# Optimization experiments

Measured on AMD Instinct MI355X. Metric: run time of the kernel, lower is better.

The kernel has to match this reference:

```python
import jax, jax.numpy as jnp
import numpy as np

P_DROP = 0.2
NEG_SLOPE = 0.2


def setup_inputs() -> dict:
    key = jax.random.key(0)
    ks = jax.random.split(key, 12)
    N, E = 50000, 800000
    IN, H1, H2, OUT = 256, 256, 128, 64
    x = jax.random.normal(ks[0], (N, IN), dtype=jnp.float32)
    adj_rows = jax.random.randint(ks[1], (E,), 0, N, dtype=jnp.int32)
    adj_cols = jax.random.randint(ks[2], (E,), 0, N, dtype=jnp.int32)
    adj_vals = jax.random.uniform(ks[3], (E,), dtype=jnp.float32)
    W1 = jax.random.normal(ks[4], (H1, IN), dtype=jnp.float32) * (1.0 / np.sqrt(IN))
    b1 = jax.random.normal(ks[5], (H1,), dtype=jnp.float32) * 0.01
    W2 = jax.random.normal(ks[6], (H2, H1), dtype=jnp.float32) * (1.0 / np.sqrt(H1))
    b2 = jax.random.normal(ks[7], (H2,), dtype=jnp.float32) * 0.01
    W3 = jax.random.normal(ks[8], (OUT, H2), dtype=jnp.float32) * (1.0 / np.sqrt(H2))
    b3 = jax.random.normal(ks[9], (OUT,), dtype=jnp.float32) * 0.01
    mask1 = jax.random.bernoulli(ks[10], 1.0 - P_DROP, (N, H1))
    mask2 = jax.random.bernoulli(ks[11], 1.0 - P_DROP, (N, H2))
    return {"x": x, "adj_rows": adj_rows, "adj_cols": adj_cols, "adj_vals": adj_vals,
            "W1": W1, "b1": b1, "W2": W2, "b2": b2, "W3": W3, "b3": b3,
            "mask1": mask1, "mask2": mask2}


def _spmm(rows, cols, vals, h, n_nodes):
    # sparse adjacency matmul: out[r] = sum_e vals[e] * h[cols[e]] for rows[e]==r
    msgs = vals[:, None] * h[cols]  # [E, d] irregular gather
    return jax.ops.segment_sum(msgs, rows, num_segments=n_nodes)


def _gcn_layer(x, W, b, rows, cols, vals, n_nodes):
    h = x @ W.T + b  # nn.Linear
    return _spmm(rows, cols, vals, h, n_nodes)


def reference(x, adj_rows, adj_cols, adj_vals, W1, b1, W2, b2, W3, b3, mask1, mask2):
    N = x.shape[0]
    keep = 1.0 / (1.0 - P_DROP)
    h = _gcn_layer(x, W1, b1, adj_rows, adj_cols, adj_vals, N)
    h = jnp.where(h >= 0, h, NEG_SLOPE * h)
    h = jnp.where(mask1, h * keep, 0.0)
    h = _gcn_layer(h, W2, b2, adj_rows, adj_cols, adj_vals, N)
    h = jnp.where(h >= 0, h, NEG_SLOPE * h)
    h = jnp.where(mask2, h * keep, 0.0)
    z = _gcn_layer(h, W3, b3, adj_rows, adj_cols, adj_vals, N)
    return z
```

## Files before the change

kernel.cpp:

```cpp
#include <hip/hip_runtime.h>


typedef unsigned short ushort_t;
typedef __attribute__((ext_vector_type(8))) short bf16x8;
typedef __attribute__((ext_vector_type(4))) float f32x4;
typedef __attribute__((ext_vector_type(2))) unsigned int u32x2;

__device__ __forceinline__ float bf2f(ushort_t u) {
  return __uint_as_float(((unsigned int)u) << 16);
}
__device__ __forceinline__ ushort_t f2bf(float f) {
  unsigned int u = __float_as_uint(f);
  return (ushort_t)((u + 0x7FFFu + ((u >> 16) & 1u)) >> 16);
}
__device__ __forceinline__ float read_f(const void* p, int fm, size_t i) {
  return fm ? bf2f(((const ushort_t*)p)[i]) : ((const float*)p)[i];
}

__device__ __forceinline__ bool mask_keep(const void* mask, int mm, size_t o) {
  switch (mm) {
    case 1:  return ((const int*)mask)[o] != 0;
    case 2:  return ((const unsigned int*)mask)[o] != 0u;
    case 3:  return ((const ushort_t*)mask)[o] != 0;
    default: return ((const unsigned char*)mask)[o] != 0;
  }
}

__global__ void prep_kernel(const void* __restrict__ x,
                            const void* __restrict__ m1,
                            const void* __restrict__ m2,
                            int* __restrict__ modes,
                            int* __restrict__ zero_region, int zn) {
  if (blockIdx.x == 0) {
    __shared__ int bfok;
    if (threadIdx.x == 0) bfok = 1;
    __syncthreads();
    for (int i = threadIdx.x; i < 8192; i += blockDim.x) {
      ushort_t h = ((const ushort_t*)x)[i];
      int e = (h >> 7) & 0xFF;
      if (!(h == 0 || (e >= 95 && e <= 133))) atomicAnd(&bfok, 0);
    }
    __syncthreads();
    if (threadIdx.x == 0) modes[0] = bfok;
  } else if (blockIdx.x <= 2) {
    const void* p = (blockIdx.x == 1) ? m1 : m2;
    __shared__ int ok[4];
    if (threadIdx.x < 4) ok[threadIdx.x] = 1;
    __syncthreads();
    for (int i = threadIdx.x; i < 4096; i += blockDim.x) {
      unsigned int w = ((const unsigned int*)p)[i];
      if (!(w == 0u || w == 1u)) atomicAnd(&ok[0], 0);
      if (!(w == 0u || w == 0x3F800000u)) atomicAnd(&ok[1], 0);
      unsigned int h16 = w >> 16, l16 = w & 0xFFFFu;
      if (!((h16 == 0u || h16 == 0x3F80u) && (l16 == 0u || l16 == 0x3F80u)))
        atomicAnd(&ok[2], 0);
      if (((w | (w >> 8) | (w >> 16) | (w >> 24)) & 0xFEu) != 0u) atomicAnd(&ok[3], 0);
    }
    __syncthreads();
    if (threadIdx.x == 0)
      modes[blockIdx.x] = ok[0] ? 1 : (ok[1] ? 2 : (ok[2] ? 3 : 0));
  } else {
    int i = (blockIdx.x - 3) * blockDim.x + threadIdx.x;
    int stride = (gridDim.x - 3) * blockDim.x;
    for (; i < zn; i += stride) zero_region[i] = 0;
  }
}

__global__ void hist_kernel(const int* __restrict__ rows, int* __restrict__ cnt, int E) {
  int i = blockIdx.x * blockDim.x + threadIdx.x;
  int stride = gridDim.x * blockDim.x;
  for (; i < E; i += stride) atomicAdd(&cnt[rows[i]], 1);
}

__global__ void scan_part_kernel(const int* __restrict__ cnt, int* __restrict__ part, int n) {
  __shared__ int s[256];
  int i = blockIdx.x * 256 + threadIdx.x;
  s[threadIdx.x] = (i < n) ? cnt[i] : 0;
  __syncthreads();
  for (int off = 128; off > 0; off >>= 1) {
    if (threadIdx.x < off) s[threadIdx.x] += s[threadIdx.x + off];
    __syncthreads();
  }
  if (threadIdx.x == 0) part[blockIdx.x] = s[0];
}

__global__ __launch_bounds__(1024) void scan_top_kernel(int* __restrict__ part, int P) {
  __shared__ int s[1024];
  int t = threadIdx.x;
  int v = (t < P) ? part[t] : 0;
  s[t] = v;
  __syncthreads();
  for (int off = 1; off < 1024; off <<= 1) {
    int x = s[t];
    int y = (t >= off) ? s[t - off] : 0;
    __syncthreads();
    s[t] = x + y;
    __syncthreads();
  }
  if (t < P) part[t] = s[t] - v;
}

__global__ void scan_apply_kernel(const int* __restrict__ cnt, const int* __restrict__ part,
                                  int* __restrict__ row_start, int n) {
  __shared__ int s[256];
  int base = part[blockIdx.x];
  int i = blockIdx.x * 256 + threadIdx.x;
  int v = (i < n) ? cnt[i] : 0;
  s[threadIdx.x] = v;
  __syncthreads();
  for (int off = 1; off < 256; off <<= 1) {
    int x = s[threadIdx.x];
    int y = (threadIdx.x >= off) ? s[threadIdx.x - off] : 0;
    __syncthreads();
    s[threadIdx.x] = x + y;
    __syncthreads();
  }
  if (i < n) row_start[i] = base + s[threadIdx.x] - v;
  if (i == n - 1) row_start[n] = base + s[threadIdx.x];
}

__global__ void scatter_kernel(const int* __restrict__ rows, const int* __restrict__ cols,
                               const void* __restrict__ vals, const int* __restrict__ fm_p,
                               const int* __restrict__ row_start, int* __restrict__ fill,
                               int2* __restrict__ ecv, int E) {
  int fm = *fm_p;
  int i = blockIdx.x * blockDim.x + threadIdx.x;
  int stride = gridDim.x * blockDim.x;
  for (; i < E; i += stride) {
    int r = rows[i];
    int pos = atomicAdd(&fill[r], 1);
    int idx = row_start[r] + pos;
    ecv[idx] = make_int2(cols[i], __float_as_int(read_f(vals, fm, i)));
  }
}

__global__ void convert_all_kernel(
    const void* __restrict__ W1, const void* __restrict__ W2, const void* __restrict__ W3,
    const void* __restrict__ b1, const void* __restrict__ b2, const void* __restrict__ b3,
    const void* __restrict__ x, const int* __restrict__ fm_p,
    ushort_t* __restrict__ whi, ushort_t* __restrict__ wlo,
    float* __restrict__ biasf, ushort_t* __restrict__ xbf,
    int n1, int n2, int n3, int h1, int h2, int h3, int nx4) {
  int fm = *fm_p;
  int wtot = n1 + n2 + n3;
  int btot = h1 + h2 + h3;
  int total = wtot + btot + nx4;
  int i = blockIdx.x * blockDim.x + threadIdx.x;
  int stride = gridDim.x * blockDim.x;
  for (; i < total; i += stride) {
    if (i < wtot) {
      const void* src; int j;
      if (i < n1) { src = W1; j = i; }
      else if (i < n1 + n2) { src = W2; j = i - n1; }
      else { src = W3; j = i - n1 - n2; }
      float v = read_f(src, fm, j);
      ushort_t h = f2bf(v);
      whi[i] = h;
      wlo[i] = f2bf(v - bf2f(h));
    } else if (i < wtot + btot) {
      int k = i - wtot;
      const void* src; int j;
      if (k < h1) { src = b1; j = k; }
      else if (k < h1 + h2) { src = b2; j = k - h1; }
      else { src = b3; j = k - h1 - h2; }
      biasf[k] = read_f(src, fm, j);
    } else {
      int k = i - wtot - btot;
      if (fm == 0) {
        f32x4 v = ((const f32x4*)x)[k];
        unsigned int lo = (unsigned int)f2bf(v[0]) | ((unsigned int)f2bf(v[1]) << 16);
        unsigned int hi = (unsigned int)f2bf(v[2]) | ((unsigned int)f2bf(v[3]) << 16);
        ((u32x2*)xbf)[k] = (u32x2){lo, hi};
      } else {
        ((u32x2*)xbf)[k] = ((const u32x2*)x)[k];
      }
    }
  }
}

template<int KC>
__global__ __launch_bounds__(256) void gemm_breg_kernel(
    const ushort_t* __restrict__ A,
    const ushort_t* __restrict__ Whi, const ushort_t* __restrict__ Wlo,
    const float* __restrict__ bias, ushort_t* __restrict__ g, int ldg,
    int M, int nct) {
  const int K = KC * 32;
  int wave = threadIdx.x >> 6, lane = threadIdx.x & 63;
  int gw = blockIdx.x * 4 + wave;
  int NW = gridDim.x * 4;
  int mr = lane & 15, quad = lane >> 4;
  int ct = gw % nct;
  int nrt = (M + 15) >> 4;
  int ntasks = nct * nrt;
  if (gw >= ntasks) return;

  bf16x8 wh[KC], wl[KC];
  {
    const ushort_t* wp = Whi + (size_t)(ct * 16 + mr) * K + quad * 8;
    const ushort_t* wq = Wlo + (size_t)(ct * 16 + mr) * K + quad * 8;
#pragma unroll
    for (int kc = 0; kc < KC; ++kc) {
      wh[kc] = *(const bf16x8*)(wp + kc * 32);
      wl[kc] = *(const bf16x8*)(wq + kc * 32);
    }
  }
  int col = ct * 16 + mr;
  float bv = bias[col];

  int task = gw;
  bf16x8 af[KC];
  {
    int m = (task / nct) * 16 + mr; if (m >= M) m = M - 1;
    const ushort_t* ap = A + (size_t)m * K + quad * 8;
#pragma unroll
    for (int kc = 0; kc < KC; ++kc) af[kc] = *(const bf16x8*)(ap + kc * 32);
  }

#pragma unroll 1
  for (;;) {
    int next = task + NW;
    bool has_next = next < ntasks;
    bf16x8 afn[KC];
    if (has_next) {
      int m = (next / nct) * 16 + mr; if (m >= M) m = M - 1;
      const ushort_t* ap = A + (size_t)m * K + quad * 8;
#pragma unroll
      for (int kc = 0; kc < KC; ++kc) afn[kc] = *(const bf16x8*)(ap + kc * 32);
    }

    f32x4 acc[4];
#pragma unroll
    for (int t = 0; t < 4; ++t) acc[t] = (f32x4){0.f, 0.f, 0.f, 0.f};
#pragma unroll
    for (int kc = 0; kc < KC; ++kc) {
      acc[(2 * kc) & 3] = __builtin_amdgcn_mfma_f32_16x16x32_bf16(af[kc], wh[kc], acc[(2 * kc) & 3], 0, 0, 0);
      acc[(2 * kc + 1) & 3] = __builtin_amdgcn_mfma_f32_16x16x32_bf16(af[kc], wl[kc], acc[(2 * kc + 1) & 3], 0, 0, 0);
    }
    int m0 = (task / nct) * 16;
#pragma unroll
    for (int r = 0; r < 4; ++r) {
      int row = m0 + quad * 4 + r;
      float s = ((acc[0][r] + acc[1][r]) + (acc[2][r] + acc[3][r])) + bv;
      if (row < M) g[(size_t)row * ldg + col] = f2bf(s);
    }
    if (!has_next) break;
#pragma unroll
    for (int kc = 0; kc < KC; ++kc) af[kc] = afn[kc];
    task = next;
  }
}

template<int MODE, int VEC>
__global__ __launch_bounds__(256) void spmm7_kernel(
    const int* __restrict__ row_start, const int2* __restrict__ ecv,
    const ushort_t* __restrict__ G, int D,
    const void* __restrict__ mask, const int* __restrict__ mmode_p,
    void* __restrict__ outp, int N) {
  int wave = threadIdx.x >> 6, lane = threadIdx.x & 63;
  int r = blockIdx.x * 4 + wave;
  if (r >= N) return;
  int f0 = lane * VEC;
  int e  = __builtin_amdgcn_readfirstlane(row_start[r]);
  int e1 = __builtin_amdgcn_readfirstlane(row_start[r + 1]);
  float a[VEC];
#pragma unroll
  for (int q = 0; q < VEC; ++q) a[q] = 0.f;

  for (; e + 8 <= e1; e += 8) {
    int2 cv[8];
#pragma unroll
    for (int j = 0; j < 8; ++j) cv[j] = ecv[e + j];
    if (VEC == 4) {
      u32x2 gg[8];
#pragma unroll
      for (int j = 0; j < 8; ++j)
        gg[j] = *(const u32x2*)(G + (size_t)cv[j].x * D + f0);
#pragma unroll
      for (int j = 0; j < 8; ++j) {
        float v = __int_as_float(cv[j].y);
        a[0] += v * bf2f((ushort_t)gg[j][0]);
        a[1] += v * bf2f((ushort_t)(gg[j][0] >> 16));
        a[2] += v * bf2f((ushort_t)gg[j][1]);
        a[3] += v * bf2f((ushort_t)(gg[j][1] >> 16));
      }
    } else if (VEC == 2) {
      unsigned int gg[8];
#pragma unroll
      for (int j = 0; j < 8; ++j)
        gg[j] = *(const unsigned int*)(G + (size_t)cv[j].x * D + f0);
#pragma unroll
      for (int j = 0; j < 8; ++j) {
        float v = __int_as_float(cv[j].y);
        a[0] += v * bf2f((ushort_t)gg[j]);
        a[1] += v * bf2f((ushort_t)(gg[j] >> 16));
      }
    } else {
      ushort_t h[8];
#pragma unroll
      for (int j = 0; j < 8; ++j) h[j] = G[(size_t)cv[j].x * D + f0];
#pragma unroll
      for (int j = 0; j < 8; ++j) a[0] += __int_as_float(cv[j].y) * bf2f(h[j]);
    }
  }
  if (e < e1) {
    int idx[8]; float v[8];
#pragma unroll
    for (int j = 0; j < 8; ++j) {
      int ee = e + j;
      bool ok = ee < e1;
      int2 cv = ecv[ok ? ee : e1 - 1];
      idx[j] = cv.x;
      v[j] = ok ? __int_as_float(cv.y) : 0.f;
    }
    if (VEC == 4) {
      u32x2 gg[8];
#pragma unroll
      for (int j = 0; j < 8; ++j)
        gg[j] = *(const u32x2*)(G + (size_t)idx[j] * D + f0);
#pragma unroll
      for (int j = 0; j < 8; ++j) {
        a[0] += v[j] * bf2f((ushort_t)gg[j][0]);
        a[1] += v[j] * bf2f((ushort_t)(gg[j][0] >> 16));
        a[2] += v[j] * bf2f((ushort_t)gg[j][1]);
        a[3] += v[j] * bf2f((ushort_t)(gg[j][1] >> 16));
      }
    } else if (VEC == 2) {
      unsigned int gg[8];
#pragma unroll
      for (int j = 0; j < 8; ++j)
        gg[j] = *(const unsigned int*)(G + (size_t)idx[j] * D + f0);
#pragma unroll
      for (int j = 0; j < 8; ++j) {
        a[0] += v[j] * bf2f((ushort_t)gg[j]);
        a[1] += v[j] * bf2f((ushort_t)(gg[j] >> 16));
      }
    } else {
      ushort_t h[8];
#pragma unroll
      for (int j = 0; j < 8; ++j) h[j] = G[(size_t)idx[j] * D + f0];
#pragma unroll
      for (int j = 0; j < 8; ++j) a[0] += v[j] * bf2f(h[j]);
    }
  }

  size_t o = (size_t)r * D + f0;
  if (MODE == 1) {
    int mm = *mmode_p;
    ushort_t pk[VEC];
#pragma unroll
    for (int q = 0; q < VEC; ++q) {
      float t = a[q];
      t = (t >= 0.f) ? t : 0.2f * t;
      t = mask_keep(mask, mm, o + q) ? t * 1.25f : 0.f;
      pk[q] = f2bf(t);
    }
    if (VEC == 4) {
      u32x2 w;
      w[0] = (unsigned int)pk[0] | ((unsigned int)pk[1] << 16);
      w[1] = (unsigned int)pk[2] | ((unsigned int)pk[3] << 16);
      *(u32x2*)((ushort_t*)outp + o) = w;
    } else if (VEC == 2) {
      *(unsigned int*)((ushort_t*)outp + o) =
          (unsigned int)pk[0] | ((unsigned int)pk[1] << 16);
    } else {
      ((ushort_t*)outp)[o] = pk[0];
    }
  } else {
#pragma unroll
    for (int q = 0; q < VEC; ++q) ((float*)outp)[o + q] = a[q];
  }
}

extern "C" void kernel_launch(void* const* d_in, const int* in_sizes, int n_in,
                              void* d_out, int out_size, void* d_ws, size_t ws_size,
                              hipStream_t stream) {
  const void* x     = d_in[0];
  const int*  rows  = (const int*)d_in[1];
  const int*  cols  = (const int*)d_in[2];
  const void* vals  = d_in[3];
  const void* W1    = d_in[4];
  const void* b1    = d_in[5];
  const void* W2    = d_in[6];
  const void* b2    = d_in[7];
  const void* W3    = d_in[8];
  const void* b3    = d_in[9];
  const void* mask1 = d_in[10];
  const void* mask2 = d_in[11];

  const int H1  = in_sizes[5];
  const int H2  = in_sizes[7];
  const int OUT = in_sizes[9];
  const int IN  = in_sizes[4] / H1;
  const int N   = in_sizes[0] / IN;
  const int E   = in_sizes[1];
  const int W1n = in_sizes[4], W2n = in_sizes[6], W3n = in_sizes[8];

  char* ws = (char*)d_ws;
  size_t off = 0;
  auto alloc = [&](size_t bytes) -> void* {
    void* p = ws + off;
    off = (off + bytes + 255) & ~(size_t)255;
    return p;
  };
  int*      modes     = (int*)alloc(4 * 4);
  int*      row_start = (int*)alloc((size_t)(N + 1) * 4);
  int*      cnt       = (int*)alloc((size_t)N * 8);
  int*      part      = (int*)alloc(1024 * 4);
  int2*     ecv       = (int2*)alloc((size_t)E * 8);
  ushort_t* whi       = (ushort_t*)alloc((size_t)(W1n + W2n + W3n) * 2);
  ushort_t* wlo       = (ushort_t*)alloc((size_t)(W1n + W2n + W3n) * 2);
  float*    biasf     = (float*)alloc((size_t)(H1 + H2 + OUT) * 4);
  ushort_t* bufA      = (ushort_t*)alloc((size_t)N * H1 * 2);
  ushort_t* bufB      = (ushort_t*)alloc((size_t)N * H1 * 2);
  ushort_t* bufC      = (ushort_t*)alloc((size_t)N * H1 * 2);

  int* fmode = modes;
  int* mm1   = modes + 1;
  int* mm2   = modes + 2;
  int* fill  = cnt + N;
  ushort_t* w1hi = whi,             *w1lo = wlo;
  ushort_t* w2hi = whi + W1n,       *w2lo = wlo + W1n;
  ushort_t* w3hi = whi + W1n + W2n, *w3lo = wlo + W1n + W2n;

  prep_kernel<<<259, 256, 0, stream>>>(x, mask1, mask2, modes, cnt, 2 * N);

  const int P = (N + 255) / 256;
  hist_kernel<<<1024, 256, 0, stream>>>(rows, cnt, E);
  scan_part_kernel<<<P, 256, 0, stream>>>(cnt, part, N);
  scan_top_kernel<<<1, 1024, 0, stream>>>(part, P);
  scan_apply_kernel<<<P, 256, 0, stream>>>(cnt, part, row_start, N);
  scatter_kernel<<<1024, 256, 0, stream>>>(rows, cols, vals, fmode, row_start, fill, ecv, E);

  convert_all_kernel<<<2048, 256, 0, stream>>>(
      W1, W2, W3, b1, b2, b3, x, fmode, whi, wlo, biasf, bufA,
      W1n, W2n, W3n, H1, H2, OUT, (N * IN) / 4);

  const int GEMM_BLOCKS = 1024;
  int spmm_grid = (N + 3) / 4;

  gemm_breg_kernel<8><<<GEMM_BLOCKS, 256, 0, stream>>>(
      bufA, w1hi, w1lo, biasf, bufB, H1, N, H1 / 16);
  spmm7_kernel<1, 4><<<spmm_grid, 256, 0, stream>>>(
      row_start, ecv, bufB, H1, mask1, mm1, bufC, N);
  gemm_breg_kernel<8><<<GEMM_BLOCKS, 256, 0, stream>>>(
      bufC, w2hi, w2lo, biasf + H1, bufB, H2, N, H2 / 16);
  spmm7_kernel<1, 2><<<spmm_grid, 256, 0, stream>>>(
      row_start, ecv, bufB, H2, mask2, mm2, bufA, N);
  gemm_breg_kernel<4><<<GEMM_BLOCKS, 256, 0, stream>>>(
      bufA, w3hi, w3lo, biasf + H1 + H2, bufB, OUT, N, OUT / 16);
  spmm7_kernel<0, 1><<<spmm_grid, 256, 0, stream>>>(
      row_start, ecv, bufB, OUT, nullptr, fmode, d_out, N);
}
```

Baseline: 477.9 us.

## Store GEMM operands in MFMA fragment-major layout for contiguous wave loads

Weights, the converted input and the SpMM outputs that feed the next GEMM are now written in a fragment-tiled layout (16-row blocks, 32-wide k chunks), so each wave loads a whole bf16x8 fragment as one contiguous 1 KB span instead of strided row reads. This is meant to make GEMM A/W loads fully coalesced. The cost is scattered, less coalesced writes in the convert and SpMM epilogues, and buffers padded to a multiple of 16 rows. Padding rows are never written, so GEMM reads uninitialised data there, but those rows are discarded at store time.

```diff
diff --git a/kernel.cpp b/kernel.cpp
--- a/kernel.cpp
+++ b/kernel.cpp
@@ -15,6 +15,11 @@
 }
 __device__ __forceinline__ float read_f(const void* p, int fm, size_t i) {
   return fm ? bf2f(((const ushort_t*)p)[i]) : ((const float*)p)[i];
+}
+
+__device__ __forceinline__ size_t frag_off(int m, int k, int K) {
+  return (size_t)(m >> 4) * 16 * K + ((size_t)(k >> 5) << 9) +
+         (((k >> 3) & 3) << 7) + ((m & 15) << 3) + (k & 7);
 }
 
 __device__ __forceinline__ bool mask_keep(const void* mask, int mm, size_t o) {
@@ -140,23 +145,26 @@
     const void* __restrict__ x, const int* __restrict__ fm_p,
     ushort_t* __restrict__ whi, ushort_t* __restrict__ wlo,
     float* __restrict__ biasf, ushort_t* __restrict__ xbf,
-    int n1, int n2, int n3, int h1, int h2, int h3, int nx4) {
+    int n1, int n2, int n3, int h1, int h2, int h3, int K1, int K2, int K3, int nx) {
   int fm = *fm_p;
   int wtot = n1 + n2 + n3;
   int btot = h1 + h2 + h3;
+  int nx4 = nx / 4;
   int total = wtot + btot + nx4;
   int i = blockIdx.x * blockDim.x + threadIdx.x;
   int stride = gridDim.x * blockDim.x;
   for (; i < total; i += stride) {
     if (i < wtot) {
-      const void* src; int j;
-      if (i < n1) { src = W1; j = i; }
-      else if (i < n1 + n2) { src = W2; j = i - n1; }
-      else { src = W3; j = i - n1 - n2; }
+      const void* src; int j, K; size_t base;
+      if (i < n1) { src = W1; j = i; K = K1; base = 0; }
+      else if (i < n1 + n2) { src = W2; j = i - n1; K = K2; base = n1; }
+      else { src = W3; j = i - n1 - n2; K = K3; base = (size_t)n1 + n2; }
+      int n = j / K, k = j - n * K;
       float v = read_f(src, fm, j);
       ushort_t h = f2bf(v);
-      whi[i] = h;
-      wlo[i] = f2bf(v - bf2f(h));
+      size_t o = base + frag_off(n, k, K);
+      whi[o] = h;
+      wlo[o] = f2bf(v - bf2f(h));
     } else if (i < wtot + btot) {
       int k = i - wtot;
       const void* src; int j;
@@ -165,15 +173,21 @@
       else { src = b3; j = k - h1 - h2; }
       biasf[k] = read_f(src, fm, j);
     } else {
-      int k = i - wtot - btot;
+      int k4 = i - wtot - btot;
+      int m = k4 / (K1 / 4);
+      int k0 = (k4 - m * (K1 / 4)) * 4;
+      ushort_t p0, p1, p2, p3;
       if (fm == 0) {
-        f32x4 v = ((const f32x4*)x)[k];
-        unsigned int lo = (unsigned int)f2bf(v[0]) | ((unsigned int)f2bf(v[1]) << 16);
-        unsigned int hi = (unsigned int)f2bf(v[2]) | ((unsigned int)f2bf(v[3]) << 16);
-        ((u32x2*)xbf)[k] = (u32x2){lo, hi};
+        f32x4 v = ((const f32x4*)x)[k4];
+        p0 = f2bf(v[0]); p1 = f2bf(v[1]); p2 = f2bf(v[2]); p3 = f2bf(v[3]);
       } else {
-        ((u32x2*)xbf)[k] = ((const u32x2*)x)[k];
+        const ushort_t* xb = (const ushort_t*)x + (size_t)k4 * 4;
+        p0 = xb[0]; p1 = xb[1]; p2 = xb[2]; p3 = xb[3];
       }
+      size_t o = frag_off(m, k0, K1);
+      *(u32x2*)(xbf + o) = (u32x2){
+          (unsigned int)p0 | ((unsigned int)p1 << 16),
+          (unsigned int)p2 | ((unsigned int)p3 << 16)};
     }
   }
 }
@@ -196,12 +210,12 @@
 
   bf16x8 wh[KC], wl[KC];
   {
-    const ushort_t* wp = Whi + (size_t)(ct * 16 + mr) * K + quad * 8;
-    const ushort_t* wq = Wlo + (size_t)(ct * 16 + mr) * K + quad * 8;
+    const ushort_t* wp = Whi + (size_t)ct * 16 * K + lane * 8;
+    const ushort_t* wq = Wlo + (size_t)ct * 16 * K + lane * 8;
 #pragma unroll
     for (int kc = 0; kc < KC; ++kc) {
-      wh[kc] = *(const bf16x8*)(wp + kc * 32);
-      wl[kc] = *(const bf16x8*)(wq + kc * 32);
+      wh[kc] = *(const bf16x8*)(wp + kc * 512);
+      wl[kc] = *(const bf16x8*)(wq + kc * 512);
     }
   }
   int col = ct * 16 + mr;
@@ -210,10 +224,9 @@
   int task = gw;
   bf16x8 af[KC];
   {
-    int m = (task / nct) * 16 + mr; if (m >= M) m = M - 1;
-    const ushort_t* ap = A + (size_t)m * K + quad * 8;
-#pragma unroll
-    for (int kc = 0; kc < KC; ++kc) af[kc] = *(const bf16x8*)(ap + kc * 32);
+    const ushort_t* ap = A + (size_t)(task / nct) * 16 * K + lane * 8;
+#pragma unroll
+    for (int kc = 0; kc < KC; ++kc) af[kc] = *(const bf16x8*)(ap + kc * 512);
   }
 
 #pragma unroll 1
@@ -222,10 +235,9 @@
     bool has_next = next < ntasks;
     bf16x8 afn[KC];
     if (has_next) {
-      int m = (next / nct) * 16 + mr; if (m >= M) m = M - 1;
-      const ushort_t* ap = A + (size_t)m * K + quad * 8;
-#pragma unroll
-      for (int kc = 0; kc < KC; ++kc) afn[kc] = *(const bf16x8*)(ap + kc * 32);
+      const ushort_t* ap = A + (size_t)(next / nct) * 16 * K + lane * 8;
+#pragma unroll
+      for (int kc = 0; kc < KC; ++kc) afn[kc] = *(const bf16x8*)(ap + kc * 512);
     }
 
     f32x4 acc[4];
@@ -343,22 +355,22 @@
     }
   }
 
-  size_t o = (size_t)r * D + f0;
   if (MODE == 1) {
+    size_t om = (size_t)r * D + f0;
     int mm = *mmode_p;
     ushort_t pk[VEC];
 #pragma unroll
     for (int q = 0; q < VEC; ++q) {
       float t = a[q];
       t = (t >= 0.f) ? t : 0.2f * t;
-      t = mask_keep(mask, mm, o + q) ? t * 1.25f : 0.f;
+      t = mask_keep(mask, mm, om + q) ? t * 1.25f : 0.f;
       pk[q] = f2bf(t);
     }
+    size_t o = frag_off(r, f0, D);
     if (VEC == 4) {
-      u32x2 w;
-      w[0] = (unsigned int)pk[0] | ((unsigned int)pk[1] << 16);
-      w[1] = (unsigned int)pk[2] | ((unsigned int)pk[3] << 16);
-      *(u32x2*)((ushort_t*)outp + o) = w;
+      *(u32x2*)((ushort_t*)outp + o) = (u32x2){
+          (unsigned int)pk[0] | ((unsigned int)pk[1] << 16),
+          (unsigned int)pk[2] | ((unsigned int)pk[3] << 16)};
     } else if (VEC == 2) {
       *(unsigned int*)((ushort_t*)outp + o) =
           (unsigned int)pk[0] | ((unsigned int)pk[1] << 16);
@@ -366,6 +378,7 @@
       ((ushort_t*)outp)[o] = pk[0];
     }
   } else {
+    size_t o = (size_t)r * D + f0;
 #pragma unroll
     for (int q = 0; q < VEC; ++q) ((float*)outp)[o + q] = a[q];
   }
@@ -394,6 +407,7 @@
   const int N   = in_sizes[0] / IN;
   const int E   = in_sizes[1];
   const int W1n = in_sizes[4], W2n = in_sizes[6], W3n = in_sizes[8];
+  const int Np  = ((N + 15) / 16) * 16;
 
   char* ws = (char*)d_ws;
   size_t off = 0;
@@ -410,9 +424,9 @@
   ushort_t* whi       = (ushort_t*)alloc((size_t)(W1n + W2n + W3n) * 2);
   ushort_t* wlo       = (ushort_t*)alloc((size_t)(W1n + W2n + W3n) * 2);
   float*    biasf     = (float*)alloc((size_t)(H1 + H2 + OUT) * 4);
-  ushort_t* bufA      = (ushort_t*)alloc((size_t)N * H1 * 2);
-  ushort_t* bufB      = (ushort_t*)alloc((size_t)N * H1 * 2);
-  ushort_t* bufC      = (ushort_t*)alloc((size_t)N * H1 * 2);
+  ushort_t* bufA      = (ushort_t*)alloc((size_t)Np * H1 * 2);
+  ushort_t* bufB      = (ushort_t*)alloc((size_t)Np * H1 * 2);
+  ushort_t* bufC      = (ushort_t*)alloc((size_t)Np * H1 * 2);
 
   int* fmode = modes;
   int* mm1   = modes + 1;
@@ -433,7 +447,7 @@
 
   convert_all_kernel<<<2048, 256, 0, stream>>>(
       W1, W2, W3, b1, b2, b3, x, fmode, whi, wlo, biasf, bufA,
-      W1n, W2n, W3n, H1, H2, OUT, (N * IN) / 4);
+      W1n, W2n, W3n, H1, H2, OUT, IN, H1, H2, N * IN);
 
   const int GEMM_BLOCKS = 1024;
   int spmm_grid = (N + 3) / 4;
```

Result: faster. 454.0 us (-5.0%).
